# Kernel optimization log

Hardware: AMD Instinct MI355X
Metric: run time of the kernel (lower is better)

The kernel has to match this reference:

```python
import jax, jax.numpy as jnp
import numpy as np

N_DEV, N_TASK, E = 50000, 100000, 1000000
F_DEV, F_TASK = 64, 64
HID, H, OUT = 16, 4, 32
L1 = HID * H  # 64


def gat_conv(x_src, x_dst, src, dst, W_src, W_dst, a_src, a_dst, b, heads, ch, n_dst):
    """PyG-style bipartite GATConv (concat=True, negative_slope=0.2, no self loops)."""
    hs = (x_src @ W_src).reshape(-1, heads, ch)          # [Ns,H,C]
    hd = (x_dst @ W_dst).reshape(-1, heads, ch)          # [Nd,H,C]
    al_s = jnp.sum(hs * a_src, axis=-1)                  # [Ns,H]
    al_d = jnp.sum(hd * a_dst, axis=-1)                  # [Nd,H]
    e = jax.nn.leaky_relu(al_s[src] + al_d[dst], 0.2)    # [E,H]
    m = jax.ops.segment_max(e, dst, num_segments=n_dst)  # [Nd,H]
    ex = jnp.exp(e - m[dst])
    den = jax.ops.segment_sum(ex, dst, num_segments=n_dst)
    attn = ex / (den[dst] + 1e-16)                       # [E,H]
    msg = attn[:, :, None] * hs[src]                     # [E,H,C]
    out = jax.ops.segment_sum(msg, dst, num_segments=n_dst)
    return out.reshape(n_dst, heads * ch) + b


def setup_inputs() -> dict:
    key = jax.random.key(0)
    ks = jax.random.split(key, 32)
    rn = lambda k, s: jax.random.normal(k, s, jnp.float32) * 0.1
    inp = {
        "x_dev": jax.random.normal(ks[0], (N_DEV, F_DEV), jnp.float32),
        "x_task": jax.random.normal(ks[1], (N_TASK, F_TASK), jnp.float32),
        "writes_src": jax.random.randint(ks[2], (E,), 0, N_DEV, jnp.int32),
        "writes_dst": jax.random.randint(ks[3], (E,), 0, N_TASK, jnp.int32),
        "wb_src": jax.random.randint(ks[4], (E,), 0, N_TASK, jnp.int32),
        "wb_dst": jax.random.randint(ks[5], (E,), 0, N_DEV, jnp.int32),
        # layer1: dev->task (src=dev, dst=task), H=4, C=16
        "W1a_src": rn(ks[6], (F_DEV, L1)), "W1a_dst": rn(ks[7], (F_TASK, L1)),
        "a1a_src": rn(ks[8], (H, HID)), "a1a_dst": rn(ks[9], (H, HID)),
        "b1a": jnp.zeros((L1,), jnp.float32),
        # layer1: task->dev
        "W1b_src": rn(ks[10], (F_TASK, L1)), "W1b_dst": rn(ks[11], (F_DEV, L1)),
        "a1b_src": rn(ks[12], (H, HID)), "a1b_dst": rn(ks[13], (H, HID)),
        "b1b": jnp.zeros((L1,), jnp.float32),
        # layer2: dev->task, heads=1, C=32
        "W2a_src": rn(ks[14], (L1, OUT)), "W2a_dst": rn(ks[15], (L1, OUT)),
        "a2a_src": rn(ks[16], (1, OUT)), "a2a_dst": rn(ks[17], (1, OUT)),
        "b2a": jnp.zeros((OUT,), jnp.float32),
        # layer2: task->dev
        "W2b_src": rn(ks[18], (L1, OUT)), "W2b_dst": rn(ks[19], (L1, OUT)),
        "a2b_src": rn(ks[20], (1, OUT)), "a2b_dst": rn(ks[21], (1, OUT)),
        "b2b": jnp.zeros((OUT,), jnp.float32),
    }
    return inp


def reference(x_dev, x_task, writes_src, writes_dst, wb_src, wb_dst,
              W1a_src, W1a_dst, a1a_src, a1a_dst, b1a,
              W1b_src, W1b_dst, a1b_src, a1b_dst, b1b,
              W2a_src, W2a_dst, a2a_src, a2a_dst, b2a,
              W2b_src, W2b_dst, a2b_src, a2b_dst, b2b):
    x_task_1 = jax.nn.relu(gat_conv(x_dev, x_task, writes_src, writes_dst,
                                    W1a_src, W1a_dst, a1a_src, a1a_dst, b1a, H, HID, N_TASK))
    x_dev_1 = jax.nn.relu(gat_conv(x_task, x_dev, wb_src, wb_dst,
                                   W1b_src, W1b_dst, a1b_src, a1b_dst, b1b, H, HID, N_DEV))
    x_task_2 = jax.nn.relu(gat_conv(x_dev_1, x_task_1, writes_src, writes_dst,
                                    W2a_src, W2a_dst, a2a_src, a2a_dst, b2a, 1, OUT, N_TASK))
    x_dev_2 = jax.nn.relu(gat_conv(x_task_1, x_dev_1, wb_src, wb_dst,
                                   W2b_src, W2b_dst, a2b_src, a2b_dst, b2b, 1, OUT, N_DEV))
    return (x_dev_2, x_task_2)
```

## Files before the change

### kernel.cpp

```cpp
#include <hip/hip_runtime.h>
#include <math.h>

#define NDEV 50000
#define NTASK 100000
#define NE 1000000
#define NBK 98
#define SH_T 10
#define SH_D 9
#define NBLK_AB 512
#define CHUNK ((NE + NBLK_AB - 1) / NBLK_AB)

typedef unsigned int uint;

__device__ inline uint bf16rn(float f) {
    uint x = __float_as_uint(f);
    return (x + 0x7fffu + ((x >> 16) & 1u)) >> 16;
}
__device__ inline uint bf16pair(float a, float b) {
    return bf16rn(a) | (bf16rn(b) << 16);
}
__device__ inline float blo(uint p) { return __uint_as_float(p << 16); }
__device__ inline float bhi(uint p) { return __uint_as_float(p & 0xffff0000u); }

__global__ void prep_weights(
    const float* __restrict__ W1a_src, const float* __restrict__ a1a_src,
    const float* __restrict__ W1a_dst, const float* __restrict__ a1a_dst,
    const float* __restrict__ W1b_src, const float* __restrict__ a1b_src,
    const float* __restrict__ W1b_dst, const float* __restrict__ a1b_dst,
    const float* __restrict__ W2a_src, const float* __restrict__ a2a_src,
    const float* __restrict__ W2a_dst, const float* __restrict__ a2a_dst,
    const float* __restrict__ W2b_src, const float* __restrict__ a2b_src,
    const float* __restrict__ W2b_dst, const float* __restrict__ a2b_dst,
    float* __restrict__ Whd1_0, float* __restrict__ Whd1_1,
    float* __restrict__ Wht1_0, float* __restrict__ Wht1_1,
    float* __restrict__ Whd2_0, float* __restrict__ Whd2_1,
    float* __restrict__ Wht2_0, float* __restrict__ Wht2_1)
{
    int f = threadIdx.x;
    if (f >= 64) return;
    for (int c = 0; c < 32; ++c) Whd1_0[f*36 + c] = W1a_src[f*64 + c];
    for (int h = 0; h < 4; ++h) {
        float s = 0.f;
        for (int c = 0; c < 16; ++c) s += W1a_src[f*64 + h*16 + c] * a1a_src[h*16 + c];
        Whd1_0[f*36 + 32 + h] = s;
    }
    for (int c = 0; c < 32; ++c) Whd1_1[f*36 + c] = W1a_src[f*64 + 32 + c];
    for (int h = 0; h < 4; ++h) {
        float s = 0.f;
        for (int c = 0; c < 16; ++c) s += W1b_dst[f*64 + h*16 + c] * a1b_dst[h*16 + c];
        Whd1_1[f*36 + 32 + h] = s;
    }
    for (int c = 0; c < 32; ++c) Wht1_0[f*36 + c] = W1b_src[f*64 + c];
    for (int h = 0; h < 4; ++h) {
        float s = 0.f;
        for (int c = 0; c < 16; ++c) s += W1b_src[f*64 + h*16 + c] * a1b_src[h*16 + c];
        Wht1_0[f*36 + 32 + h] = s;
    }
    for (int c = 0; c < 32; ++c) Wht1_1[f*36 + c] = W1b_src[f*64 + 32 + c];
    for (int h = 0; h < 4; ++h) {
        float s = 0.f;
        for (int c = 0; c < 16; ++c) s += W1a_dst[f*64 + h*16 + c] * a1a_dst[h*16 + c];
        Wht1_1[f*36 + 32 + h] = s;
    }
    for (int c = 0; c < 16; ++c) Whd2_0[f*20 + c] = W2a_src[f*32 + c];
    { float s = 0.f; for (int c = 0; c < 32; ++c) s += W2a_src[f*32+c]*a2a_src[c]; Whd2_0[f*20+16] = s; }
    Whd2_0[f*20+17] = 0.f; Whd2_0[f*20+18] = 0.f; Whd2_0[f*20+19] = 0.f;
    for (int c = 0; c < 16; ++c) Whd2_1[f*20 + c] = W2a_src[f*32 + 16 + c];
    { float s = 0.f; for (int c = 0; c < 32; ++c) s += W2b_dst[f*32+c]*a2b_dst[c]; Whd2_1[f*20+16] = s; }
    Whd2_1[f*20+17] = 0.f; Whd2_1[f*20+18] = 0.f; Whd2_1[f*20+19] = 0.f;
    for (int c = 0; c < 16; ++c) Wht2_0[f*20 + c] = W2b_src[f*32 + c];
    { float s = 0.f; for (int c = 0; c < 32; ++c) s += W2b_src[f*32+c]*a2b_src[c]; Wht2_0[f*20+16] = s; }
    Wht2_0[f*20+17] = 0.f; Wht2_0[f*20+18] = 0.f; Wht2_0[f*20+19] = 0.f;
    for (int c = 0; c < 16; ++c) Wht2_1[f*20 + c] = W2b_src[f*32 + 16 + c];
    { float s = 0.f; for (int c = 0; c < 32; ++c) s += W2a_dst[f*32+c]*a2a_dst[c]; Wht2_1[f*20+16] = s; }
    Wht2_1[f*20+17] = 0.f; Wht2_1[f*20+18] = 0.f; Wht2_1[f*20+19] = 0.f;
}

template<int COP, int CHS, int NA, int AST, int HSTR>
__device__ __forceinline__ void gemm_half_block(
    const float* __restrict__ X, int N, const float* __restrict__ Wc,
    uint* __restrict__ hs, float* __restrict__ aout,
    int n0, int hsoff, float* w)
{
    for (int i = threadIdx.x; i < 64 * COP; i += 256) w[i] = Wc[i];
    __syncthreads();
    int n = n0 + threadIdx.x;
    if (n >= N) return;

    const float4* X4 = reinterpret_cast<const float4*>(X + (size_t)n * 64);
    float4 acc[CHS/4];
    #pragma unroll
    for (int j = 0; j < CHS/4; ++j) acc[j] = make_float4(0.f, 0.f, 0.f, 0.f);
    float aacc[NA];
    #pragma unroll
    for (int j = 0; j < NA; ++j) aacc[j] = 0.f;

    for (int k16 = 0; k16 < 4; ++k16) {
        float4 xv4[4];
        #pragma unroll
        for (int q = 0; q < 4; ++q) xv4[q] = X4[k16*4 + q];
        float xs[16];
        #pragma unroll
        for (int q = 0; q < 4; ++q) {
            xs[4*q+0] = xv4[q].x; xs[4*q+1] = xv4[q].y;
            xs[4*q+2] = xv4[q].z; xs[4*q+3] = xv4[q].w;
        }
        #pragma unroll
        for (int kk = 0; kk < 16; ++kk) {
            int k = k16*16 + kk;
            float xv = xs[kk];
            const float* wr = &w[k * COP];
            #pragma unroll
            for (int j = 0; j < CHS/4; ++j) {
                float4 wv = *reinterpret_cast<const float4*>(wr + 4*j);
                acc[j].x += xv * wv.x; acc[j].y += xv * wv.y;
                acc[j].z += xv * wv.z; acc[j].w += xv * wv.w;
            }
            #pragma unroll
            for (int j = 0; j < NA; ++j) aacc[j] += xv * wr[CHS + j];
        }
    }
    uint pk[CHS/2];
    #pragma unroll
    for (int j = 0; j < CHS/4; ++j) {
        pk[2*j]   = bf16pair(acc[j].x, acc[j].y);
        pk[2*j+1] = bf16pair(acc[j].z, acc[j].w);
    }
    uint4* hrow = reinterpret_cast<uint4*>(hs + (size_t)n * HSTR + hsoff);
    #pragma unroll
    for (int j = 0; j < CHS/8; ++j)
        hrow[j] = make_uint4(pk[4*j], pk[4*j+1], pk[4*j+2], pk[4*j+3]);
    #pragma unroll
    for (int j = 0; j < NA; ++j) aout[(size_t)n*AST + j] = aacc[j];
}

template<int COP, int CHS, int NA, int AST, int HSTR>
__global__ __launch_bounds__(256, 4) void gemm_quad(
    const float* __restrict__ XA, int NrA,
    const float* __restrict__ WcA0, const float* __restrict__ WcA1,
    uint* __restrict__ hsA, float* __restrict__ alsA, float* __restrict__ aldA,
    const float* __restrict__ XB, int NrB,
    const float* __restrict__ WcB0, const float* __restrict__ WcB1,
    uint* __restrict__ hsB, float* __restrict__ alsB, float* __restrict__ aldB)
{
    __shared__ __align__(16) float w[64 * COP];
    int nbA = (NrA + 255) / 256;
    int nbB = (NrB + 255) / 256;
    int nbHalf = nbA + nbB;
    int b = (int)blockIdx.x;
    int half = b >= nbHalf ? 1 : 0;
    if (half) b -= nbHalf;
    int isB = b >= nbA ? 1 : 0;
    if (isB) b -= nbA;
    const float* X = isB ? XB : XA;
    int N = isB ? NrB : NrA;
    const float* Wc = isB ? (half ? WcB1 : WcB0) : (half ? WcA1 : WcA0);
    uint* hs = isB ? hsB : hsA;
    float* aout = isB ? (half ? aldB : alsB) : (half ? aldA : alsA);
    gemm_half_block<COP, CHS, NA, AST, HSTR>(X, N, Wc, hs, aout, b * 256, half * (CHS/2), w);
}

__global__ __launch_bounds__(256) void bucketA(
    const int* __restrict__ wdst, const int* __restrict__ bdst,
    int* __restrict__ bh_t, int* __restrict__ bh_d)
{
    __shared__ int lh[128];
    int dir = (int)blockIdx.x >= NBLK_AB;
    int blk = (int)blockIdx.x - (dir ? NBLK_AB : 0);
    const int* dst = dir ? bdst : wdst;
    int sh = dir ? SH_D : SH_T;
    int* bh = dir ? bh_d : bh_t;
    for (int i = threadIdx.x; i < 128; i += 256) lh[i] = 0;
    __syncthreads();
    int e0 = blk * CHUNK, e1 = min(NE, e0 + CHUNK);
    for (int i = e0 + threadIdx.x; i < e1; i += 256)
        atomicAdd(&lh[dst[i] >> sh], 1);
    __syncthreads();
    if (threadIdx.x < NBK) bh[threadIdx.x * NBLK_AB + blk] = lh[threadIdx.x];
}

__global__ __launch_bounds__(256) void scanB1(
    int* __restrict__ bh_t, int* __restrict__ bh_d, int* __restrict__ rowtot)
{
    __shared__ int sm[256];
    int b = blockIdx.x;
    int dir = b >= NBK;
    int row = dir ? b - NBK : b;
    int* bh = dir ? bh_d : bh_t;
    int t = threadIdx.x;
    int base = row * NBLK_AB;
    int v0 = bh[base + 2*t], v1 = bh[base + 2*t + 1];
    int s = v0 + v1;
    sm[t] = s; __syncthreads();
    int x = s;
    for (int off = 1; off < 256; off <<= 1) {
        int y = (t >= off) ? sm[t - off] : 0;
        __syncthreads();
        x += y; sm[t] = x;
        __syncthreads();
    }
    int run = x - s;
    bh[base + 2*t] = run;
    bh[base + 2*t + 1] = run + v0;
    if (t == 255) rowtot[b] = x;
}

__global__ void scanB2(const int* __restrict__ rowtot,
                       int* __restrict__ coarse_t, int* __restrict__ coarse_d,
                       int* __restrict__ offs_task, int* __restrict__ offs_dev)
{
    __shared__ int sm[256];
    int t = threadIdx.x;
    int v = (t < NBK) ? rowtot[t] : 0;
    sm[t] = v; __syncthreads();
    int x = v;
    for (int off = 1; off < 256; off <<= 1) {
        int y = (t >= off) ? sm[t - off] : 0;
        __syncthreads();
        x += y; sm[t] = x;
        __syncthreads();
    }
    if (t < NBK) coarse_t[t] = x - v;
    __syncthreads();
    int v2 = (t < NBK) ? rowtot[NBK + t] : 0;
    sm[t] = v2; __syncthreads();
    int x2 = v2;
    for (int off = 1; off < 256; off <<= 1) {
        int y = (t >= off) ? sm[t - off] : 0;
        __syncthreads();
        x2 += y; sm[t] = x2;
        __syncthreads();
    }
    if (t < NBK) coarse_d[t] = x2 - v2;
    if (t == 0) {
        coarse_t[NBK] = NE; coarse_d[NBK] = NE;
        offs_task[NTASK] = NE; offs_dev[NDEV] = NE;
    }
}

__global__ __launch_bounds__(256) void bucketB(
    const int* __restrict__ wsrc, const int* __restrict__ wdst,
    const int* __restrict__ bsrc, const int* __restrict__ bdst,
    const int* __restrict__ bh_t, const int* __restrict__ bh_d,
    const int* __restrict__ coarse_t, const int* __restrict__ coarse_d,
    uint* __restrict__ pairs_w, uint* __restrict__ pairs_b)
{
    __shared__ int cur[128];
    int dir = (int)blockIdx.x >= NBLK_AB;
    int blk = (int)blockIdx.x - (dir ? NBLK_AB : 0);
    const int* src = dir ? bsrc : wsrc;
    const int* dst = dir ? bdst : wdst;
    int sh = dir ? SH_D : SH_T;
    uint msk = (1u << sh) - 1u;
    const int* bh = dir ? bh_d : bh_t;
    const int* coarse = dir ? coarse_d : coarse_t;
    uint* pairs = dir ? pairs_b : pairs_w;
    if (threadIdx.x < NBK)
        cur[threadIdx.x] = bh[threadIdx.x * NBLK_AB + blk] + coarse[threadIdx.x];
    __syncthreads();
    int e0 = blk * CHUNK, e1 = min(NE, e0 + CHUNK);
    for (int i = e0 + threadIdx.x; i < e1; i += 256) {
        int d = dst[i];
        int pos = atomicAdd(&cur[d >> sh], 1);
        pairs[pos] = (uint)src[i] | (((uint)d & msk) << 20);
    }
}

__global__ __launch_bounds__(256) void bucketC(
    const uint* __restrict__ pairs_w, const int* __restrict__ coarse_t,
    int* __restrict__ offs_task, int* __restrict__ s_w,
    const uint* __restrict__ pairs_b, const int* __restrict__ coarse_d,
    int* __restrict__ offs_dev, int* __restrict__ s_b)
{
    __shared__ int loff[1024];
    __shared__ int sm[256];
    int dir = (int)blockIdx.x >= NBK;
    int bkt = (int)blockIdx.x - (dir ? NBK : 0);
    const uint* pairs = dir ? pairs_b : pairs_w;
    const int* coarse = dir ? coarse_d : coarse_t;
    int* offs = dir ? offs_dev : offs_task;
    int* sarr = dir ? s_b : s_w;
    int sh = dir ? SH_D : SH_T;
    int rng = 1 << sh;
    int d0 = bkt << sh;
    int N = dir ? NDEV : NTASK;
    int dcnt = min(rng, N - d0);
    int e0 = coarse[bkt], e1 = coarse[bkt + 1];
    int t = threadIdx.x;
    for (int i = t; i < rng; i += 256) loff[i] = 0;
    __syncthreads();
    for (int i = e0 + t; i < e1; i += 256)
        atomicAdd(&loff[pairs[i] >> 20], 1);
    __syncthreads();
    int per = rng >> 8;
    int v[4]; int s = 0;
    for (int k = 0; k < per; ++k) { v[k] = loff[t * per + k]; s += v[k]; }
    sm[t] = s;
    __syncthreads();
    int x = s;
    for (int off = 1; off < 256; off <<= 1) {
        int y = (t >= off) ? sm[t - off] : 0;
        __syncthreads();
        x += y; sm[t] = x;
        __syncthreads();
    }
    int run = e0 + x - s;
    for (int k = 0; k < per; ++k) {
        int dl = t * per + k;
        loff[dl] = run;
        if (dl < dcnt) offs[d0 + dl] = run;
        run += v[k];
    }
    __syncthreads();
    for (int i = e0 + t; i < e1; i += 256) {
        uint u = pairs[i];
        int pos = atomicAdd(&loff[u >> 20], 1);
        sarr[pos] = (int)(u & 0xFFFFFu);
    }
}

__global__ __launch_bounds__(256) void gat_agg_l1(
    const int* __restrict__ offs_t, const int* __restrict__ srcs_t,
    const float* __restrict__ als_d_, const float* __restrict__ ald_t,
    const uint* __restrict__ hs_d_, const float* __restrict__ bias_a, float* __restrict__ out_t,
    const int* __restrict__ offs_d, const int* __restrict__ srcs_d,
    const float* __restrict__ als_t, const float* __restrict__ ald_d,
    const uint* __restrict__ hs_t, const float* __restrict__ bias_b, float* __restrict__ out_d)
{
    const int nbT = (NTASK + 3) / 4;
    int wave = threadIdx.x >> 6, lane = threadIdx.x & 63;
    const int* offs; const int* srcs; const float* als; const float* ald;
    const uint* hs; const float* bias; float* out; int Nd, d;
    if ((int)blockIdx.x < nbT) {
        offs = offs_t; srcs = srcs_t; als = als_d_; ald = ald_t; hs = hs_d_;
        bias = bias_a; out = out_t; Nd = NTASK; d = blockIdx.x * 4 + wave;
    } else {
        offs = offs_d; srcs = srcs_d; als = als_t; ald = ald_d; hs = hs_t;
        bias = bias_b; out = out_d; Nd = NDEV; d = ((int)blockIdx.x - nbT) * 4 + wave;
    }
    if (d >= Nd) return;
    int sub = lane >> 4;
    int cl  = lane & 15;
    int h   = cl >> 2;
    float aldv = ald[d * 4 + h];
    int beg = __builtin_amdgcn_readfirstlane(offs[d]);
    int end = __builtin_amdgcn_readfirstlane(offs[d + 1]);
    float denA = 0.f, a0A = 0.f, a1A = 0.f, a2A = 0.f, a3A = 0.f;
    float denB = 0.f, a0B = 0.f, a1B = 0.f, a2B = 0.f, a3B = 0.f;
    for (int i0 = beg + sub; i0 < end; i0 += 8) {
        int iB = i0 + 4;
        bool vB = iB < end;
        int sA = srcs[i0];
        int sB = srcs[vB ? iB : beg];
        float eA = als[sA * 4 + h] + aldv; eA = fmaxf(eA, 0.2f * eA);
        float eB = als[sB * 4 + h] + aldv; eB = fmaxf(eB, 0.2f * eB);
        float wA = __expf(eA);
        float wB = vB ? __expf(eB) : 0.f;
        uint2 pA = *reinterpret_cast<const uint2*>(hs + sA * 32 + 2 * cl);
        uint2 pB = *reinterpret_cast<const uint2*>(hs + sB * 32 + 2 * cl);
        denA += wA;
        a0A += wA * blo(pA.x); a1A += wA * bhi(pA.x);
        a2A += wA * blo(pA.y); a3A += wA * bhi(pA.y);
        denB += wB;
        a0B += wB * blo(pB.x); a1B += wB * bhi(pB.x);
        a2B += wB * blo(pB.y); a3B += wB * bhi(pB.y);
    }
    float den = denA + denB;
    float a0 = a0A + a0B, a1 = a1A + a1B, a2 = a2A + a2B, a3 = a3A + a3B;
    den += __shfl_xor(den, 16, 64); den += __shfl_xor(den, 32, 64);
    a0  += __shfl_xor(a0, 16, 64);  a0  += __shfl_xor(a0, 32, 64);
    a1  += __shfl_xor(a1, 16, 64);  a1  += __shfl_xor(a1, 32, 64);
    a2  += __shfl_xor(a2, 16, 64);  a2  += __shfl_xor(a2, 32, 64);
    a3  += __shfl_xor(a3, 16, 64);  a3  += __shfl_xor(a3, 32, 64);
    if (lane < 16) {
        float inv = 1.f / (den + 1e-16f);
        float4 o;
        o.x = fmaxf(a0 * inv + bias[4*cl + 0], 0.f);
        o.y = fmaxf(a1 * inv + bias[4*cl + 1], 0.f);
        o.z = fmaxf(a2 * inv + bias[4*cl + 2], 0.f);
        o.w = fmaxf(a3 * inv + bias[4*cl + 3], 0.f);
        *reinterpret_cast<float4*>(&out[(size_t)d * 64 + 4*cl]) = o;
    }
}

__global__ __launch_bounds__(256) void gat_agg_l2(
    const int* __restrict__ offs_t, const int* __restrict__ srcs_t,
    const float* __restrict__ als_d_, const float* __restrict__ ald_t,
    const uint* __restrict__ hs_d_, const float* __restrict__ bias_a, float* __restrict__ out_t,
    const int* __restrict__ offs_d, const int* __restrict__ srcs_d,
    const float* __restrict__ als_t, const float* __restrict__ ald_d,
    const uint* __restrict__ hs_t, const float* __restrict__ bias_b, float* __restrict__ out_d)
{
    const int nbT = (NTASK + 3) / 4;
    int wave = threadIdx.x >> 6, lane = threadIdx.x & 63;
    const int* offs; const int* srcs; const float* als; const float* ald;
    const uint* hs; const float* bias; float* out; int Nd, d;
    if ((int)blockIdx.x < nbT) {
        offs = offs_t; srcs = srcs_t; als = als_d_; ald = ald_t; hs = hs_d_;
        bias = bias_a; out = out_t; Nd = NTASK; d = blockIdx.x * 4 + wave;
    } else {
        offs = offs_d; srcs = srcs_d; als = als_t; ald = ald_d; hs = hs_t;
        bias = bias_b; out = out_d; Nd = NDEV; d = ((int)blockIdx.x - nbT) * 4 + wave;
    }
    if (d >= Nd) return;
    int sub = lane >> 3;
    int cl  = lane & 7;
    float aldv = ald[d];
    int beg = __builtin_amdgcn_readfirstlane(offs[d]);
    int end = __builtin_amdgcn_readfirstlane(offs[d + 1]);
    float denA = 0.f, a0A = 0.f, a1A = 0.f, a2A = 0.f, a3A = 0.f;
    float denB = 0.f, a0B = 0.f, a1B = 0.f, a2B = 0.f, a3B = 0.f;
    for (int i0 = beg + sub; i0 < end; i0 += 16) {
        int iB = i0 + 8;
        bool vB = iB < end;
        int sA = srcs[i0];
        int sB = srcs[vB ? iB : beg];
        float eA = als[sA] + aldv; eA = fmaxf(eA, 0.2f * eA);
        float eB = als[sB] + aldv; eB = fmaxf(eB, 0.2f * eB);
        float wA = __expf(eA);
        float wB = vB ? __expf(eB) : 0.f;
        uint2 pA = *reinterpret_cast<const uint2*>(hs + sA * 16 + 2 * cl);
        uint2 pB = *reinterpret_cast<const uint2*>(hs + sB * 16 + 2 * cl);
        denA += wA;
        a0A += wA * blo(pA.x); a1A += wA * bhi(pA.x);
        a2A += wA * blo(pA.y); a3A += wA * bhi(pA.y);
        denB += wB;
        a0B += wB * blo(pB.x); a1B += wB * bhi(pB.x);
        a2B += wB * blo(pB.y); a3B += wB * bhi(pB.y);
    }
    float den = denA + denB;
    float a0 = a0A + a0B, a1 = a1A + a1B, a2 = a2A + a2B, a3 = a3A + a3B;
    den += __shfl_xor(den, 8, 64); den += __shfl_xor(den, 16, 64); den += __shfl_xor(den, 32, 64);
    a0  += __shfl_xor(a0, 8, 64);  a0  += __shfl_xor(a0, 16, 64);  a0  += __shfl_xor(a0, 32, 64);
    a1  += __shfl_xor(a1, 8, 64);  a1  += __shfl_xor(a1, 16, 64);  a1  += __shfl_xor(a1, 32, 64);
    a2  += __shfl_xor(a2, 8, 64);  a2  += __shfl_xor(a2, 16, 64);  a2  += __shfl_xor(a2, 32, 64);
    a3  += __shfl_xor(a3, 8, 64);  a3  += __shfl_xor(a3, 16, 64);  a3  += __shfl_xor(a3, 32, 64);
    if (lane < 8) {
        float inv = 1.f / (den + 1e-16f);
        float4 o;
        o.x = fmaxf(a0 * inv + bias[4*cl + 0], 0.f);
        o.y = fmaxf(a1 * inv + bias[4*cl + 1], 0.f);
        o.z = fmaxf(a2 * inv + bias[4*cl + 2], 0.f);
        o.w = fmaxf(a3 * inv + bias[4*cl + 3], 0.f);
        *reinterpret_cast<float4*>(&out[(size_t)d * 32 + 4*cl]) = o;
    }
}

extern "C" void kernel_launch(void* const* d_in, const int* in_sizes, int n_in,
                              void* d_out, int out_size, void* d_ws, size_t ws_size,
                              hipStream_t stream)
{
    const float* x_dev   = (const float*)d_in[0];
    const float* x_task  = (const float*)d_in[1];
    const int* writes_src = (const int*)d_in[2];
    const int* writes_dst = (const int*)d_in[3];
    const int* wb_src     = (const int*)d_in[4];
    const int* wb_dst     = (const int*)d_in[5];
    const float* W1a_src = (const float*)d_in[6],  *W1a_dst = (const float*)d_in[7];
    const float* a1a_src = (const float*)d_in[8],  *a1a_dst = (const float*)d_in[9];
    const float* b1a     = (const float*)d_in[10];
    const float* W1b_src = (const float*)d_in[11], *W1b_dst = (const float*)d_in[12];
    const float* a1b_src = (const float*)d_in[13], *a1b_dst = (const float*)d_in[14];
    const float* b1b     = (const float*)d_in[15];
    const float* W2a_src = (const float*)d_in[16], *W2a_dst = (const float*)d_in[17];
    const float* a2a_src = (const float*)d_in[18], *a2a_dst = (const float*)d_in[19];
    const float* b2a     = (const float*)d_in[20];
    const float* W2b_src = (const float*)d_in[21], *W2b_dst = (const float*)d_in[22];
    const float* a2b_src = (const float*)d_in[23], *a2b_dst = (const float*)d_in[24];
    const float* b2b     = (const float*)d_in[25];

    float* out_dev2  = (float*)d_out;
    float* out_task2 = (float*)d_out + (size_t)NDEV * 32;

    char* ws = (char*)d_ws;
    size_t off = 0;
    auto take = [&](size_t bytes) -> void* {
        off = (off + 255) & ~(size_t)255;
        void* p = ws + off; off += bytes; return p;
    };
    int* s_w       = (int*)take((size_t)NE * 4);
    int* s_b       = (int*)take((size_t)NE * 4);
    int* offs_task = (int*)take((size_t)(NTASK + 1) * 4);
    int* offs_dev  = (int*)take((size_t)(NDEV + 1) * 4);
    int* bh_t      = (int*)take((size_t)NBK * NBLK_AB * 4);
    int* bh_d      = (int*)take((size_t)NBK * NBLK_AB * 4);
    int* coarse_t  = (int*)take((size_t)(NBK + 1) * 4);
    int* coarse_d  = (int*)take((size_t)(NBK + 1) * 4);
    int* rowtot    = (int*)take(256 * 4);
    float* Whd1_0  = (float*)take(64 * 36 * 4);
    float* Whd1_1  = (float*)take(64 * 36 * 4);
    float* Wht1_0  = (float*)take(64 * 36 * 4);
    float* Wht1_1  = (float*)take(64 * 36 * 4);
    float* Whd2_0  = (float*)take(64 * 20 * 4);
    float* Whd2_1  = (float*)take(64 * 20 * 4);
    float* Wht2_0  = (float*)take(64 * 20 * 4);
    float* Wht2_1  = (float*)take(64 * 20 * 4);
    uint* hs_dev    = (uint*)take((size_t)NDEV * 32 * 4);
    float* als_dev  = (float*)take((size_t)NDEV * 4 * 4);
    float* aldx_dev = (float*)take((size_t)NDEV * 4 * 4);
    uint* hs_task   = (uint*)take((size_t)NTASK * 32 * 4);
    float* als_task = (float*)take((size_t)NTASK * 4 * 4);
    float* aldx_task= (float*)take((size_t)NTASK * 4 * 4);
    float* x_task1  = (float*)take((size_t)NTASK * 64 * 4);
    float* x_dev1   = (float*)take((size_t)NDEV * 64 * 4);
    uint* pairs_w = (uint*)x_task1;
    uint* pairs_b = pairs_w + NE;
    (void)ws_size; (void)n_in; (void)in_sizes; (void)out_size;

    prep_weights<<<1, 64, 0, stream>>>(
        W1a_src, a1a_src, W1a_dst, a1a_dst, W1b_src, a1b_src, W1b_dst, a1b_dst,
        W2a_src, a2a_src, W2a_dst, a2a_dst, W2b_src, a2b_src, W2b_dst, a2b_dst,
        Whd1_0, Whd1_1, Wht1_0, Wht1_1, Whd2_0, Whd2_1, Wht2_0, Wht2_1);

    bucketA<<<2 * NBLK_AB, 256, 0, stream>>>(writes_dst, wb_dst, bh_t, bh_d);
    scanB1<<<2 * NBK, 256, 0, stream>>>(bh_t, bh_d, rowtot);
    scanB2<<<1, 256, 0, stream>>>(rowtot, coarse_t, coarse_d, offs_task, offs_dev);
    bucketB<<<2 * NBLK_AB, 256, 0, stream>>>(writes_src, writes_dst, wb_src, wb_dst,
                                             bh_t, bh_d, coarse_t, coarse_d, pairs_w, pairs_b);
    bucketC<<<2 * NBK, 256, 0, stream>>>(pairs_w, coarse_t, offs_task, s_w,
                                         pairs_b, coarse_d, offs_dev, s_b);

    int nbHalf = (NDEV + 255) / 256 + (NTASK + 255) / 256;
    gemm_quad<36, 32, 4, 4, 32><<<2 * nbHalf, 256, 0, stream>>>(
        x_dev, NDEV, Whd1_0, Whd1_1, hs_dev, als_dev, aldx_dev,
        x_task, NTASK, Wht1_0, Wht1_1, hs_task, als_task, aldx_task);

    int nbagg = (NTASK + 3) / 4 + (NDEV + 3) / 4;
    gat_agg_l1<<<nbagg, 256, 0, stream>>>(
        offs_task, s_w, als_dev, aldx_task, hs_dev, b1a, x_task1,
        offs_dev, s_b, als_task, aldx_dev, hs_task, b1b, x_dev1);

    gemm_quad<20, 16, 1, 1, 16><<<2 * nbHalf, 256, 0, stream>>>(
        x_dev1, NDEV, Whd2_0, Whd2_1, hs_dev, als_dev, aldx_dev,
        x_task1, NTASK, Wht2_0, Wht2_1, hs_task, als_task, aldx_task);

    gat_agg_l2<<<nbagg, 256, 0, stream>>>(
        offs_task, s_w, als_dev, aldx_task, hs_dev, b2a, out_task2,
        offs_dev, s_b, als_task, aldx_dev, hs_task, b2b, out_dev2);
}
```

Measured before the change: 260.1 us.

## Store layer-1 outputs as bf16 and unroll aggregation loops four ways

```diff
diff --git a/kernel.cpp b/kernel.cpp
--- a/kernel.cpp
+++ b/kernel.cpp
@@ -135,6 +135,61 @@
 }
 
 template<int COP, int CHS, int NA, int AST, int HSTR>
+__device__ __forceinline__ void gemm_half_block_b16(
+    const uint* __restrict__ X, int N, const float* __restrict__ Wc,
+    uint* __restrict__ hs, float* __restrict__ aout,
+    int n0, int hsoff, float* w)
+{
+    for (int i = threadIdx.x; i < 64 * COP; i += 256) w[i] = Wc[i];
+    __syncthreads();
+    int n = n0 + threadIdx.x;
+    if (n >= N) return;
+
+    const uint4* X4 = reinterpret_cast<const uint4*>(X + (size_t)n * 32);
+    float4 acc[CHS/4];
+    #pragma unroll
+    for (int j = 0; j < CHS/4; ++j) acc[j] = make_float4(0.f, 0.f, 0.f, 0.f);
+    float aacc[NA];
+    #pragma unroll
+    for (int j = 0; j < NA; ++j) aacc[j] = 0.f;
+
+    for (int k16 = 0; k16 < 4; ++k16) {
+        uint4 u0 = X4[2*k16], u1 = X4[2*k16 + 1];
+        float xs[16];
+        xs[0] = blo(u0.x); xs[1] = bhi(u0.x); xs[2] = blo(u0.y); xs[3] = bhi(u0.y);
+        xs[4] = blo(u0.z); xs[5] = bhi(u0.z); xs[6] = blo(u0.w); xs[7] = bhi(u0.w);
+        xs[8] = blo(u1.x); xs[9] = bhi(u1.x); xs[10] = blo(u1.y); xs[11] = bhi(u1.y);
+        xs[12] = blo(u1.z); xs[13] = bhi(u1.z); xs[14] = blo(u1.w); xs[15] = bhi(u1.w);
+        #pragma unroll
+        for (int kk = 0; kk < 16; ++kk) {
+            int k = k16*16 + kk;
+            float xv = xs[kk];
+            const float* wr = &w[k * COP];
+            #pragma unroll
+            for (int j = 0; j < CHS/4; ++j) {
+                float4 wv = *reinterpret_cast<const float4*>(wr + 4*j);
+                acc[j].x += xv * wv.x; acc[j].y += xv * wv.y;
+                acc[j].z += xv * wv.z; acc[j].w += xv * wv.w;
+            }
+            #pragma unroll
+            for (int j = 0; j < NA; ++j) aacc[j] += xv * wr[CHS + j];
+        }
+    }
+    uint pk[CHS/2];
+    #pragma unroll
+    for (int j = 0; j < CHS/4; ++j) {
+        pk[2*j]   = bf16pair(acc[j].x, acc[j].y);
+        pk[2*j+1] = bf16pair(acc[j].z, acc[j].w);
+    }
+    uint4* hrow = reinterpret_cast<uint4*>(hs + (size_t)n * HSTR + hsoff);
+    #pragma unroll
+    for (int j = 0; j < CHS/8; ++j)
+        hrow[j] = make_uint4(pk[4*j], pk[4*j+1], pk[4*j+2], pk[4*j+3]);
+    #pragma unroll
+    for (int j = 0; j < NA; ++j) aout[(size_t)n*AST + j] = aacc[j];
+}
+
+template<int COP, int CHS, int NA, int AST, int HSTR>
 __global__ __launch_bounds__(256, 4) void gemm_quad(
     const float* __restrict__ XA, int NrA,
     const float* __restrict__ WcA0, const float* __restrict__ WcA1,
@@ -158,6 +213,32 @@
     uint* hs = isB ? hsB : hsA;
     float* aout = isB ? (half ? aldB : alsB) : (half ? aldA : alsA);
     gemm_half_block<COP, CHS, NA, AST, HSTR>(X, N, Wc, hs, aout, b * 256, half * (CHS/2), w);
+}
+
+template<int COP, int CHS, int NA, int AST, int HSTR>
+__global__ __launch_bounds__(256, 4) void gemm_quad_b16(
+    const uint* __restrict__ XA, int NrA,
+    const float* __restrict__ WcA0, const float* __restrict__ WcA1,
+    uint* __restrict__ hsA, float* __restrict__ alsA, float* __restrict__ aldA,
+    const uint* __restrict__ XB, int NrB,
+    const float* __restrict__ WcB0, const float* __restrict__ WcB1,
+    uint* __restrict__ hsB, float* __restrict__ alsB, float* __restrict__ aldB)
+{
+    __shared__ __align__(16) float w[64 * COP];
+    int nbA = (NrA + 255) / 256;
+    int nbB = (NrB + 255) / 256;
+    int nbHalf = nbA + nbB;
+    int b = (int)blockIdx.x;
+    int half = b >= nbHalf ? 1 : 0;
+    if (half) b -= nbHalf;
+    int isB = b >= nbA ? 1 : 0;
+    if (isB) b -= nbA;
+    const uint* X = isB ? XB : XA;
+    int N = isB ? NrB : NrA;
+    const float* Wc = isB ? (half ? WcB1 : WcB0) : (half ? WcA1 : WcA0);
+    uint* hs = isB ? hsB : hsA;
+    float* aout = isB ? (half ? aldB : alsB) : (half ? aldA : alsA);
+    gemm_half_block_b16<COP, CHS, NA, AST, HSTR>(X, N, Wc, hs, aout, b * 256, half * (CHS/2), w);
 }
 
 __global__ __launch_bounds__(256) void bucketA(
@@ -322,6 +403,91 @@
 __global__ __launch_bounds__(256) void gat_agg_l1(
     const int* __restrict__ offs_t, const int* __restrict__ srcs_t,
     const float* __restrict__ als_d_, const float* __restrict__ ald_t,
+    const uint* __restrict__ hs_d_, const float* __restrict__ bias_a, uint* __restrict__ out_t,
+    const int* __restrict__ offs_d, const int* __restrict__ srcs_d,
+    const float* __restrict__ als_t, const float* __restrict__ ald_d,
+    const uint* __restrict__ hs_t, const float* __restrict__ bias_b, uint* __restrict__ out_d)
+{
+    const int nbT = (NTASK + 3) / 4;
+    int wave = threadIdx.x >> 6, lane = threadIdx.x & 63;
+    const int* offs; const int* srcs; const float* als; const float* ald;
+    const uint* hs; const float* bias; uint* out; int Nd, d;
+    if ((int)blockIdx.x < nbT) {
+        offs = offs_t; srcs = srcs_t; als = als_d_; ald = ald_t; hs = hs_d_;
+        bias = bias_a; out = out_t; Nd = NTASK; d = blockIdx.x * 4 + wave;
+    } else {
+        offs = offs_d; srcs = srcs_d; als = als_t; ald = ald_d; hs = hs_t;
+        bias = bias_b; out = out_d; Nd = NDEV; d = ((int)blockIdx.x - nbT) * 4 + wave;
+    }
+    if (d >= Nd) return;
+    int sub = lane >> 4;
+    int cl  = lane & 15;
+    int h   = cl >> 2;
+    float aldv = ald[d * 4 + h];
+    int beg = __builtin_amdgcn_readfirstlane(offs[d]);
+    int end = __builtin_amdgcn_readfirstlane(offs[d + 1]);
+    float denA = 0.f, a0A = 0.f, a1A = 0.f, a2A = 0.f, a3A = 0.f;
+    float denB = 0.f, a0B = 0.f, a1B = 0.f, a2B = 0.f, a3B = 0.f;
+    float denC = 0.f, a0C = 0.f, a1C = 0.f, a2C = 0.f, a3C = 0.f;
+    float denD = 0.f, a0D = 0.f, a1D = 0.f, a2D = 0.f, a3D = 0.f;
+    for (int i0 = beg + sub; i0 < end; i0 += 16) {
+        int iB = i0 + 4, iC = i0 + 8, iD = i0 + 12;
+        bool vB = iB < end, vC = iC < end, vD = iD < end;
+        int sA = srcs[i0];
+        int sB = srcs[vB ? iB : beg];
+        int sC = srcs[vC ? iC : beg];
+        int sD = srcs[vD ? iD : beg];
+        float eA = als[sA * 4 + h] + aldv; eA = fmaxf(eA, 0.2f * eA);
+        float eB = als[sB * 4 + h] + aldv; eB = fmaxf(eB, 0.2f * eB);
+        float eC = als[sC * 4 + h] + aldv; eC = fmaxf(eC, 0.2f * eC);
+        float eD = als[sD * 4 + h] + aldv; eD = fmaxf(eD, 0.2f * eD);
+        float wA = __expf(eA);
+        float wB = vB ? __expf(eB) : 0.f;
+        float wC = vC ? __expf(eC) : 0.f;
+        float wD = vD ? __expf(eD) : 0.f;
+        uint2 pA = *reinterpret_cast<const uint2*>(hs + sA * 32 + 2 * cl);
+        uint2 pB = *reinterpret_cast<const uint2*>(hs + sB * 32 + 2 * cl);
+        uint2 pC = *reinterpret_cast<const uint2*>(hs + sC * 32 + 2 * cl);
+        uint2 pD = *reinterpret_cast<const uint2*>(hs + sD * 32 + 2 * cl);
+        denA += wA;
+        a0A += wA * blo(pA.x); a1A += wA * bhi(pA.x);
+        a2A += wA * blo(pA.y); a3A += wA * bhi(pA.y);
+        denB += wB;
+        a0B += wB * blo(pB.x); a1B += wB * bhi(pB.x);
+        a2B += wB * blo(pB.y); a3B += wB * bhi(pB.y);
+        denC += wC;
+        a0C += wC * blo(pC.x); a1C += wC * bhi(pC.x);
+        a2C += wC * blo(pC.y); a3C += wC * bhi(pC.y);
+        denD += wD;
+        a0D += wD * blo(pD.x); a1D += wD * bhi(pD.x);
+        a2D += wD * blo(pD.y); a3D += wD * bhi(pD.y);
+    }
+    float den = (denA + denB) + (denC + denD);
+    float a0 = (a0A + a0B) + (a0C + a0D);
+    float a1 = (a1A + a1B) + (a1C + a1D);
+    float a2 = (a2A + a2B) + (a2C + a2D);
+    float a3 = (a3A + a3B) + (a3C + a3D);
+    den += __shfl_xor(den, 16, 64); den += __shfl_xor(den, 32, 64);
+    a0  += __shfl_xor(a0, 16, 64);  a0  += __shfl_xor(a0, 32, 64);
+    a1  += __shfl_xor(a1, 16, 64);  a1  += __shfl_xor(a1, 32, 64);
+    a2  += __shfl_xor(a2, 16, 64);  a2  += __shfl_xor(a2, 32, 64);
+    a3  += __shfl_xor(a3, 16, 64);  a3  += __shfl_xor(a3, 32, 64);
+    if (lane < 16) {
+        float inv = 1.f / (den + 1e-16f);
+        float o0 = fmaxf(a0 * inv + bias[4*cl + 0], 0.f);
+        float o1 = fmaxf(a1 * inv + bias[4*cl + 1], 0.f);
+        float o2 = fmaxf(a2 * inv + bias[4*cl + 2], 0.f);
+        float o3 = fmaxf(a3 * inv + bias[4*cl + 3], 0.f);
+        uint2 pk;
+        pk.x = bf16pair(o0, o1);
+        pk.y = bf16pair(o2, o3);
+        *reinterpret_cast<uint2*>(&out[(size_t)d * 32 + 2*cl]) = pk;
+    }
+}
+
+__global__ __launch_bounds__(256) void gat_agg_l2(
+    const int* __restrict__ offs_t, const int* __restrict__ srcs_t,
+    const float* __restrict__ als_d_, const float* __restrict__ ald_t,
     const uint* __restrict__ hs_d_, const float* __restrict__ bias_a, float* __restrict__ out_t,
     const int* __restrict__ offs_d, const int* __restrict__ srcs_d,
     const float* __restrict__ als_t, const float* __restrict__ ald_d,
@@ -339,70 +505,6 @@
         bias = bias_b; out = out_d; Nd = NDEV; d = ((int)blockIdx.x - nbT) * 4 + wave;
     }
     if (d >= Nd) return;
-    int sub = lane >> 4;
-    int cl  = lane & 15;
-    int h   = cl >> 2;
-    float aldv = ald[d * 4 + h];
-    int beg = __builtin_amdgcn_readfirstlane(offs[d]);
-    int end = __builtin_amdgcn_readfirstlane(offs[d + 1]);
-    float denA = 0.f, a0A = 0.f, a1A = 0.f, a2A = 0.f, a3A = 0.f;
-    float denB = 0.f, a0B = 0.f, a1B = 0.f, a2B = 0.f, a3B = 0.f;
-    for (int i0 = beg + sub; i0 < end; i0 += 8) {
-        int iB = i0 + 4;
-        bool vB = iB < end;
-        int sA = srcs[i0];
-        int sB = srcs[vB ? iB : beg];
-        float eA = als[sA * 4 + h] + aldv; eA = fmaxf(eA, 0.2f * eA);
-        float eB = als[sB * 4 + h] + aldv; eB = fmaxf(eB, 0.2f * eB);
-        float wA = __expf(eA);
-        float wB = vB ? __expf(eB) : 0.f;
-        uint2 pA = *reinterpret_cast<const uint2*>(hs + sA * 32 + 2 * cl);
-        uint2 pB = *reinterpret_cast<const uint2*>(hs + sB * 32 + 2 * cl);
-        denA += wA;
-        a0A += wA * blo(pA.x); a1A += wA * bhi(pA.x);
-        a2A += wA * blo(pA.y); a3A += wA * bhi(pA.y);
-        denB += wB;
-        a0B += wB * blo(pB.x); a1B += wB * bhi(pB.x);
-        a2B += wB * blo(pB.y); a3B += wB * bhi(pB.y);
-    }
-    float den = denA + denB;
-    float a0 = a0A + a0B, a1 = a1A + a1B, a2 = a2A + a2B, a3 = a3A + a3B;
-    den += __shfl_xor(den, 16, 64); den += __shfl_xor(den, 32, 64);
-    a0  += __shfl_xor(a0, 16, 64);  a0  += __shfl_xor(a0, 32, 64);
-    a1  += __shfl_xor(a1, 16, 64);  a1  += __shfl_xor(a1, 32, 64);
-    a2  += __shfl_xor(a2, 16, 64);  a2  += __shfl_xor(a2, 32, 64);
-    a3  += __shfl_xor(a3, 16, 64);  a3  += __shfl_xor(a3, 32, 64);
-    if (lane < 16) {
-        float inv = 1.f / (den + 1e-16f);
-        float4 o;
-        o.x = fmaxf(a0 * inv + bias[4*cl + 0], 0.f);
-        o.y = fmaxf(a1 * inv + bias[4*cl + 1], 0.f);
-        o.z = fmaxf(a2 * inv + bias[4*cl + 2], 0.f);
-        o.w = fmaxf(a3 * inv + bias[4*cl + 3], 0.f);
-        *reinterpret_cast<float4*>(&out[(size_t)d * 64 + 4*cl]) = o;
-    }
-}
-
-__global__ __launch_bounds__(256) void gat_agg_l2(
-    const int* __restrict__ offs_t, const int* __restrict__ srcs_t,
-    const float* __restrict__ als_d_, const float* __restrict__ ald_t,
-    const uint* __restrict__ hs_d_, const float* __restrict__ bias_a, float* __restrict__ out_t,
-    const int* __restrict__ offs_d, const int* __restrict__ srcs_d,
-    const float* __restrict__ als_t, const float* __restrict__ ald_d,
-    const uint* __restrict__ hs_t, const float* __restrict__ bias_b, float* __restrict__ out_d)
-{
-    const int nbT = (NTASK + 3) / 4;
-    int wave = threadIdx.x >> 6, lane = threadIdx.x & 63;
-    const int* offs; const int* srcs; const float* als; const float* ald;
-    const uint* hs; const float* bias; float* out; int Nd, d;
-    if ((int)blockIdx.x < nbT) {
-        offs = offs_t; srcs = srcs_t; als = als_d_; ald = ald_t; hs = hs_d_;
-        bias = bias_a; out = out_t; Nd = NTASK; d = blockIdx.x * 4 + wave;
-    } else {
-        offs = offs_d; srcs = srcs_d; als = als_t; ald = ald_d; hs = hs_t;
-        bias = bias_b; out = out_d; Nd = NDEV; d = ((int)blockIdx.x - nbT) * 4 + wave;
-    }
-    if (d >= Nd) return;
     int sub = lane >> 3;
     int cl  = lane & 7;
     float aldv = ald[d];
@@ -410,26 +512,45 @@
     int end = __builtin_amdgcn_readfirstlane(offs[d + 1]);
     float denA = 0.f, a0A = 0.f, a1A = 0.f, a2A = 0.f, a3A = 0.f;
     float denB = 0.f, a0B = 0.f, a1B = 0.f, a2B = 0.f, a3B = 0.f;
-    for (int i0 = beg + sub; i0 < end; i0 += 16) {
-        int iB = i0 + 8;
-        bool vB = iB < end;
+    float denC = 0.f, a0C = 0.f, a1C = 0.f, a2C = 0.f, a3C = 0.f;
+    float denD = 0.f, a0D = 0.f, a1D = 0.f, a2D = 0.f, a3D = 0.f;
+    for (int i0 = beg + sub; i0 < end; i0 += 32) {
+        int iB = i0 + 8, iC = i0 + 16, iD = i0 + 24;
+        bool vB = iB < end, vC = iC < end, vD = iD < end;
         int sA = srcs[i0];
         int sB = srcs[vB ? iB : beg];
+        int sC = srcs[vC ? iC : beg];
+        int sD = srcs[vD ? iD : beg];
         float eA = als[sA] + aldv; eA = fmaxf(eA, 0.2f * eA);
         float eB = als[sB] + aldv; eB = fmaxf(eB, 0.2f * eB);
+        float eC = als[sC] + aldv; eC = fmaxf(eC, 0.2f * eC);
+        float eD = als[sD] + aldv; eD = fmaxf(eD, 0.2f * eD);
         float wA = __expf(eA);
         float wB = vB ? __expf(eB) : 0.f;
+        float wC = vC ? __expf(eC) : 0.f;
+        float wD = vD ? __expf(eD) : 0.f;
         uint2 pA = *reinterpret_cast<const uint2*>(hs + sA * 16 + 2 * cl);
         uint2 pB = *reinterpret_cast<const uint2*>(hs + sB * 16 + 2 * cl);
+        uint2 pC = *reinterpret_cast<const uint2*>(hs + sC * 16 + 2 * cl);
+        uint2 pD = *reinterpret_cast<const uint2*>(hs + sD * 16 + 2 * cl);
         denA += wA;
         a0A += wA * blo(pA.x); a1A += wA * bhi(pA.x);
         a2A += wA * blo(pA.y); a3A += wA * bhi(pA.y);
         denB += wB;
         a0B += wB * blo(pB.x); a1B += wB * bhi(pB.x);
         a2B += wB * blo(pB.y); a3B += wB * bhi(pB.y);
-    }
-    float den = denA + denB;
-    float a0 = a0A + a0B, a1 = a1A + a1B, a2 = a2A + a2B, a3 = a3A + a3B;
+        denC += wC;
+        a0C += wC * blo(pC.x); a1C += wC * bhi(pC.x);
+        a2C += wC * blo(pC.y); a3C += wC * bhi(pC.y);
+        denD += wD;
+        a0D += wD * blo(pD.x); a1D += wD * bhi(pD.x);
+        a2D += wD * blo(pD.y); a3D += wD * bhi(pD.y);
+    }
+    float den = (denA + denB) + (denC + denD);
+    float a0 = (a0A + a0B) + (a0C + a0D);
+    float a1 = (a1A + a1B) + (a1C + a1D);
+    float a2 = (a2A + a2B) + (a2C + a2D);
+    float a3 = (a3A + a3B) + (a3C + a3D);
     den += __shfl_xor(den, 8, 64); den += __shfl_xor(den, 16, 64); den += __shfl_xor(den, 32, 64);
     a0  += __shfl_xor(a0, 8, 64);  a0  += __shfl_xor(a0, 16, 64);  a0  += __shfl_xor(a0, 32, 64);
     a1  += __shfl_xor(a1, 8, 64);  a1  += __shfl_xor(a1, 16, 64);  a1  += __shfl_xor(a1, 32, 64);
@@ -501,8 +622,8 @@
     uint* hs_task   = (uint*)take((size_t)NTASK * 32 * 4);
     float* als_task = (float*)take((size_t)NTASK * 4 * 4);
     float* aldx_task= (float*)take((size_t)NTASK * 4 * 4);
-    float* x_task1  = (float*)take((size_t)NTASK * 64 * 4);
-    float* x_dev1   = (float*)take((size_t)NDEV * 64 * 4);
+    uint* x_task1   = (uint*)take((size_t)NTASK * 32 * 4);
+    uint* x_dev1    = (uint*)take((size_t)NDEV * 32 * 4);
     uint* pairs_w = (uint*)x_task1;
     uint* pairs_b = pairs_w + NE;
     (void)ws_size; (void)n_in; (void)in_sizes; (void)out_size;
@@ -530,7 +651,7 @@
         offs_task, s_w, als_dev, aldx_task, hs_dev, b1a, x_task1,
         offs_dev, s_b, als_task, aldx_dev, hs_task, b1b, x_dev1);
 
-    gemm_quad<20, 16, 1, 1, 16><<<2 * nbHalf, 256, 0, stream>>>(
+    gemm_quad_b16<20, 16, 1, 1, 16><<<2 * nbHalf, 256, 0, stream>>>(
         x_dev1, NDEV, Whd2_0, Whd2_1, hs_dev, als_dev, aldx_dev,
         x_task1, NTASK, Wht2_0, Wht2_1, hs_task, als_task, aldx_task);
 
```

Result: faster. 243.8 us (-6.3%).
